# Kernel optimization log

Measured on AMD Instinct MI355X. Metric: run time of the kernel, lower is better.

Reference implementation:

```python
import jax, jax.numpy as jnp
import numpy as np

N_HEAD, N, F_IN, F_OUT = 8, 4096, 128, 128


def setup_inputs() -> dict:
    key = jax.random.key(0)
    k1, k2, k3, k4 = jax.random.split(key, 4)
    return {
        "h": jax.random.normal(k1, (N, F_IN), dtype=jnp.float32),
        "w": jax.random.normal(k2, (N_HEAD, F_IN, F_OUT), dtype=jnp.float32) * 0.1,
        "a_src": jax.random.normal(k3, (N_HEAD, F_OUT, 1), dtype=jnp.float32) * 0.1,
        "a_dst": jax.random.normal(k4, (N_HEAD, F_OUT, 1), dtype=jnp.float32) * 0.1,
        "bias": jnp.zeros((F_OUT,), dtype=jnp.float32),
        "idx": 0,
    }


def reference(h, w, a_src, a_dst, bias, idx):
    # h: [n, f_in], w: [H, f_in, f_out] -> h_prime: [H, n, f_out]
    h_prime = jnp.einsum("ni,hio->hno", h, w)
    # per-node scalar scores per head: [H, n]
    attn_src = jnp.einsum("hno,ho->hn", h_prime, a_src[..., 0])
    attn_dst = jnp.einsum("hno,ho->hn", h_prime, a_dst[..., 0])
    # dense additive attention: [H, n, n] (src broadcast over cols + dst over rows)
    attn = attn_src[:, :, None] + attn_dst[:, None, :]
    attn = jax.nn.leaky_relu(attn, negative_slope=0.2)
    attn = jax.nn.softmax(attn, axis=-1)
    # dropout is identity in eval mode
    out = jnp.einsum("hnm,hmo->hno", attn, h_prime)  # [H, n, f_out]
    return out.mean(axis=0) + bias  # [n, f_out]
```

## Files before the change

### kernel.cpp

```cpp
#include <hip/hip_runtime.h>
#include <math.h>

#define NH 8
#define NN 4096
#define FF 128
#define SEG 32
#define NSEG (NN / SEG)

typedef unsigned long long u64;

__global__ __launch_bounds__(128) void kA_va(
    const float* __restrict__ w, const float* __restrict__ a_src,
    const float* __restrict__ a_dst, float* __restrict__ va_s,
    float* __restrict__ va_d) {
  __shared__ float as[FF], ad[FF];
  const int head = blockIdx.x, i = threadIdx.x;
  as[i] = a_src[head * FF + i];
  ad[i] = a_dst[head * FF + i];
  __syncthreads();
  const float4* wr = reinterpret_cast<const float4*>(w + (size_t)head * FF * FF +
                                                     (size_t)i * FF);
  float s = 0.f, d = 0.f;
  #pragma unroll 8
  for (int q = 0; q < 32; ++q) {
    float4 v = wr[q];
    s += v.x * as[q * 4] + v.y * as[q * 4 + 1] + v.z * as[q * 4 + 2] +
         v.w * as[q * 4 + 3];
    d += v.x * ad[q * 4] + v.y * ad[q * 4 + 1] + v.z * ad[q * 4 + 2] +
         v.w * ad[q * 4 + 3];
  }
  va_s[head * FF + i] = s;
  va_d[head * FF + i] = d;
}

__global__ __launch_bounds__(256) void kB_scores(
    const float* __restrict__ h, const float* __restrict__ va_s,
    const float* __restrict__ va_d, float* __restrict__ attn_src,
    float* __restrict__ attn_dst) {
  __shared__ float sh[32 * 132];
  __shared__ float vs[NH * 132], vd[NH * 132];
  const int r0 = blockIdx.x * 32;
  const int tid = threadIdx.x;
  const float4* hg = reinterpret_cast<const float4*>(h);
  #pragma unroll
  for (int it = 0; it < 4; ++it) {
    int q = tid + it * 256;
    int row = q >> 5, c4 = q & 31;
    float4 v = hg[(size_t)(r0 + row) * 32 + c4];
    float* dst = &sh[row * 132 + c4 * 4];
    dst[0] = v.x; dst[1] = v.y; dst[2] = v.z; dst[3] = v.w;
  }
  for (int q = tid; q < NH * FF; q += 256) {
    int hd = q >> 7, k = q & 127;
    vs[hd * 132 + k] = va_s[q];
    vd[hd * 132 + k] = va_d[q];
  }
  __syncthreads();
  const int row = tid >> 3, head = tid & 7;
  float s = 0.f, d = 0.f;
  const float* hr = &sh[row * 132];
  const float* vsp = &vs[head * 132];
  const float* vdp = &vd[head * 132];
  #pragma unroll 8
  for (int k = 0; k < FF; ++k) {
    float hv = hr[k];
    s += hv * vsp[k];
    d += hv * vdp[k];
  }
  attn_src[head * NN + r0 + row] = s;
  attn_dst[head * NN + r0 + row] = d;
}

__global__ __launch_bounds__(256) void k2a_localsort(
    const float* __restrict__ adst, u64* __restrict__ runs) {
  __shared__ u64 sk[512];
  const int head = blockIdx.y, chunk = blockIdx.x, tid = threadIdx.x;
  const int base = head * NN + chunk * 512;
  for (int i = tid; i < 512; i += 256) {
    unsigned ub = __float_as_uint(adst[base + i]);
    unsigned u = (ub & 0x80000000u) ? ~ub : (ub | 0x80000000u);
    sk[i] = ((u64)u << 32) | (unsigned)(chunk * 512 + i);
  }
  __syncthreads();
  for (int k = 2; k <= 512; k <<= 1) {
    for (int j = k >> 1; j > 0; j >>= 1) {
      for (int t = tid; t < 512; t += 256) {
        int ixj = t ^ j;
        if (ixj > t) {
          u64 a = sk[t], b = sk[ixj];
          bool up = ((t & k) == 0);
          if (up ? (a > b) : (a < b)) { sk[t] = b; sk[ixj] = a; }
        }
      }
      __syncthreads();
    }
  }
  for (int i = tid; i < 512; i += 256) runs[base + i] = sk[i];
}

template <int L, bool FINAL>
__global__ __launch_bounds__(256) void k2m(
    const u64* __restrict__ src, u64* __restrict__ dst,
    float* __restrict__ dsort, int* __restrict__ permd) {
  const int head = blockIdx.y;
  const int i = (blockIdx.x * 256 + threadIdx.x) * 4;
  const u64* S = src + head * NN;
  const int region = i / (2 * L), q0 = i % (2 * L);
  const u64* A = S + region * 2 * L;
  const u64* B = A + L;
  int lo = q0 > L ? q0 - L : 0, hi = q0 < L ? q0 : L;
  while (lo < hi) {
    int mid = (lo + hi) >> 1;
    if (A[mid] < B[q0 - 1 - mid]) lo = mid + 1; else hi = mid;
  }
  int a = lo, b = q0 - lo;
  #pragma unroll
  for (int t = 0; t < 4; ++t) {
    u64 va = a < L ? A[a] : ~0ULL;
    u64 vb = b < L ? B[b] : ~0ULL;
    u64 v;
    if (va < vb) { v = va; ++a; } else { v = vb; ++b; }
    const int q = region * 2 * L + q0 + t;
    if (FINAL) {
      unsigned u = (unsigned)(v >> 32);
      unsigned ub = (u & 0x80000000u) ? (u ^ 0x80000000u) : ~u;
      dsort[head * NN + q] = __uint_as_float(ub);
      permd[head * NN + q] = (int)(v & 0xffffffffu);
    } else {
      dst[head * NN + q] = v;
    }
  }
}

__global__ __launch_bounds__(256) void kD_gemm_seg(
    const float* __restrict__ h, const float* __restrict__ w,
    const float* __restrict__ dsort, const int* __restrict__ permd,
    float* __restrict__ hs, float* __restrict__ segs,
    float* __restrict__ segz) {
  __shared__ float sw[32 * 128];
  __shared__ float hA[32 * 128];
  __shared__ float red[2 * 8 * 128];
  __shared__ float se0[SEG], se1[SEG];
  __shared__ int sp[SEG];
  const int head = blockIdx.y, seg = blockIdx.x;
  const int tid = threadIdx.x;
  const int ty = tid >> 5, tx = tid & 31;
  if (tid < SEG) {
    float dv = dsort[head * NN + seg * SEG + tid];
    se0[tid] = expf(0.2f * dv);
    se1[tid] = expf(dv);
    sp[tid] = permd[head * NN + seg * SEG + tid];
  }
  __syncthreads();
  const float4* hg = reinterpret_cast<const float4*>(h);
  #pragma unroll
  for (int it = 0; it < 4; ++it) {
    int row = tid >> 3, c4 = (tid & 7) + it * 8;
    float4 v = hg[(size_t)sp[row] * 32 + c4];
    float* dst = &hA[row * 128 + c4 * 4];
    dst[0] = v.x; dst[1] = v.y; dst[2] = v.z; dst[3] = v.w;
  }
  float acc[4][4];
  #pragma unroll
  for (int i = 0; i < 4; ++i)
    #pragma unroll
    for (int j = 0; j < 4; ++j) acc[i][j] = 0.f;
  const float4* wg = reinterpret_cast<const float4*>(w + (size_t)head * FF * FF);
  for (int kc = 0; kc < 4; ++kc) {
    const int k0 = kc * 32;
    __syncthreads();
    #pragma unroll
    for (int it = 0; it < 4; ++it) {
      int q = tid + it * 256;
      int krow = q >> 5, c4 = q & 31;
      float4 v = wg[(size_t)(k0 + krow) * 32 + c4];
      float* dst = &sw[krow * 128 + c4 * 4];
      dst[0] = v.x; dst[1] = v.y; dst[2] = v.z; dst[3] = v.w;
    }
    __syncthreads();
    #pragma unroll 8
    for (int kk = 0; kk < 32; ++kk) {
      float4 b4 = *reinterpret_cast<const float4*>(&sw[kk * 128 + tx * 4]);
      #pragma unroll
      for (int ri = 0; ri < 4; ++ri) {
        float av = hA[(ty * 4 + ri) * 128 + k0 + kk];
        acc[ri][0] += av * b4.x;
        acc[ri][1] += av * b4.y;
        acc[ri][2] += av * b4.z;
        acc[ri][3] += av * b4.w;
      }
    }
  }
  float4* hs4 = reinterpret_cast<float4*>(hs);
  #pragma unroll
  for (int ri = 0; ri < 4; ++ri) {
    hs4[((size_t)(head * NN + seg * SEG + ty * 4 + ri)) * 32 + tx] =
        make_float4(acc[ri][0], acc[ri][1], acc[ri][2], acc[ri][3]);
  }
  #pragma unroll
  for (int c = 0; c < 4; ++c) {
    float p0 = 0.f, p1 = 0.f;
    #pragma unroll
    for (int ri = 0; ri < 4; ++ri) {
      int R = ty * 4 + ri;
      p0 += se0[R] * acc[ri][c];
      p1 += se1[R] * acc[ri][c];
    }
    red[ty * 128 + tx * 4 + c] = p0;
    red[1024 + ty * 128 + tx * 4 + c] = p1;
  }
  __syncthreads();
  if (tid < FF) {
    float a0 = 0.f, a1 = 0.f;
    #pragma unroll
    for (int g = 0; g < 8; ++g) {
      a0 += red[g * 128 + tid];
      a1 += red[1024 + g * 128 + tid];
    }
    size_t base = ((size_t)(head * NSEG + seg)) * 2 * FF;
    segs[base + tid] = a0;
    segs[base + FF + tid] = a1;
  }
  if (tid == 0) {
    float z0 = 0.f, z1 = 0.f;
    #pragma unroll
    for (int j = 0; j < SEG; ++j) { z0 += se0[j]; z1 += se1[j]; }
    segz[(head * NSEG + seg) * 2 + 0] = z0;
    segz[(head * NSEG + seg) * 2 + 1] = z1;
  }
}

__global__ __launch_bounds__(256) void k4_thresh(
    const float* __restrict__ attn_src, const float* __restrict__ dsort,
    int* __restrict__ tpos) {
  const int i = blockIdx.x * 256 + threadIdx.x;
  const int head = i >> 12, n = i & (NN - 1);
  const float thr = -attn_src[head * NN + n];
  const float* dp = dsort + head * NN;
  int lo = 0, hi = NN;
  while (lo < hi) {
    int mid = (lo + hi) >> 1;
    if (dp[mid] <= thr) lo = mid + 1; else hi = mid;
  }
  tpos[i] = lo;
}

__global__ __launch_bounds__(128) void kF_prefix(
    const float* __restrict__ hs, const float* __restrict__ dsort,
    const float* __restrict__ segs, const float* __restrict__ segz,
    float* __restrict__ PF, float* __restrict__ PFz) {
  __shared__ float se0[SEG], se1[SEG];
  const int head = blockIdx.y, seg = blockIdx.x;
  const int o = threadIdx.x;
  if (o < SEG) {
    float dv = dsort[head * NN + seg * SEG + o];
    se0[o] = expf(0.2f * dv);
    se1[o] = expf(dv);
  }
  __syncthreads();
  float r0 = 0.f, r1 = 0.f, z0 = 0.f, z1 = 0.f;
  const float* sbase = segs + ((size_t)head * NSEG) * 2 * FF;
  #pragma unroll 8
  for (int k = 0; k < seg; ++k) {
    r0 += sbase[(size_t)k * 2 * FF + o];
    r1 += sbase[(size_t)k * 2 * FF + FF + o];
  }
  #pragma unroll 8
  for (int k = 0; k < seg; ++k) {
    z0 += segz[(head * NSEG + k) * 2 + 0];
    z1 += segz[(head * NSEG + k) * 2 + 1];
  }
  const float* hrow = hs + ((size_t)(head * NN + seg * SEG)) * FF + o;
  #pragma unroll 8
  for (int jj = 0; jj < SEG; ++jj) {
    int j = seg * SEG + jj;
    float hv = hrow[(size_t)jj * FF];
    float e0 = se0[jj], e1 = se1[jj];
    r0 += e0 * hv;
    r1 += e1 * hv;
    z0 += e0;
    z1 += e1;
    size_t pb = ((size_t)(head * NN + j)) * 2 * FF;
    PF[pb + o] = r0;
    PF[pb + FF + o] = r1;
    if (o == 0) {
      PFz[(head * NN + j) * 2 + 0] = z0;
      PFz[(head * NN + j) * 2 + 1] = z1;
    }
  }
}

__global__ __launch_bounds__(128) void k6_out(
    const float* __restrict__ attn_src, const int* __restrict__ tpos,
    const float* __restrict__ PF, const float* __restrict__ PFz,
    const float* __restrict__ bias, float* __restrict__ out) {
  const int n = blockIdx.x, o = threadIdx.x;
  float acc = 0.f;
  #pragma unroll
  for (int head = 0; head < NH; ++head) {
    float s = attn_src[head * NN + n];
    int t = tpos[head * NN + n];
    size_t tb = ((size_t)(head * NN + NN - 1)) * 2 * FF;
    float TotA = PF[tb + FF + o];
    float z1tot = PFz[(head * NN + NN - 1) * 2 + 1];
    float B = 0.f, P1 = 0.f, z0p = 0.f, z1p = 0.f;
    if (t > 0) {
      size_t pb = ((size_t)(head * NN + t - 1)) * 2 * FF;
      B = PF[pb + o];
      P1 = PF[pb + FF + o];
      z0p = PFz[(head * NN + t - 1) * 2 + 0];
      z1p = PFz[(head * NN + t - 1) * 2 + 1];
    }
    float e02s = expf(0.2f * s), es = expf(s);
    float den = e02s * z0p + es * (z1tot - z1p);
    acc += (e02s * B + es * (TotA - P1)) / den;
  }
  out[(size_t)n * FF + o] = 0.125f * acc + bias[o];
}

extern "C" void kernel_launch(void* const* d_in, const int* in_sizes, int n_in,
                              void* d_out, int out_size, void* d_ws,
                              size_t ws_size, hipStream_t stream) {
  const float* h = (const float*)d_in[0];
  const float* w = (const float*)d_in[1];
  const float* a_src = (const float*)d_in[2];
  const float* a_dst = (const float*)d_in[3];
  const float* bias = (const float*)d_in[4];
  float* out = (float*)d_out;

  char* ws = (char*)d_ws;
  size_t off = 0;
  auto alloc = [&](size_t bytes) -> void* {
    void* p = ws + off;
    off += (bytes + 255) & ~(size_t)255;
    return p;
  };
  float* hs = (float*)alloc((size_t)NH * NN * FF * 4);
  float* va_s = (float*)alloc((size_t)NH * FF * 4);
  float* va_d = (float*)alloc((size_t)NH * FF * 4);
  float* asrc = (float*)alloc((size_t)NH * NN * 4);
  float* adst = (float*)alloc((size_t)NH * NN * 4);
  float* dsort = (float*)alloc((size_t)NH * NN * 4);
  int* permd = (int*)alloc((size_t)NH * NN * 4);
  int* tpos = (int*)alloc((size_t)NH * NN * 4);
  float* segs = (float*)alloc((size_t)NH * NSEG * 2 * FF * 4);
  float* segz = (float*)alloc((size_t)NH * NSEG * 2 * 4);
  float* PF = (float*)alloc((size_t)NH * NN * 2 * FF * 4);
  float* PFz = (float*)alloc((size_t)NH * NN * 2 * 4);
  u64* sbuf0 = (u64*)alloc((size_t)NH * NN * 8);
  u64* sbuf1 = (u64*)alloc((size_t)NH * NN * 8);
  (void)ws_size; (void)in_sizes; (void)n_in;

  kA_va<<<NH, 128, 0, stream>>>(w, a_src, a_dst, va_s, va_d);
  kB_scores<<<NN / 32, 256, 0, stream>>>(h, va_s, va_d, asrc, adst);
  k2a_localsort<<<dim3(8, NH), 256, 0, stream>>>(adst, sbuf0);
  k2m<512, false><<<dim3(4, NH), 256, 0, stream>>>(sbuf0, sbuf1, nullptr,
                                                   nullptr);
  k2m<1024, false><<<dim3(4, NH), 256, 0, stream>>>(sbuf1, sbuf0, nullptr,
                                                    nullptr);
  k2m<2048, true><<<dim3(4, NH), 256, 0, stream>>>(sbuf0, nullptr, dsort,
                                                   permd);
  kD_gemm_seg<<<dim3(NSEG, NH), 256, 0, stream>>>(h, w, dsort, permd, hs, segs,
                                                  segz);
  k4_thresh<<<NH * NN / 256, 256, 0, stream>>>(asrc, dsort, tpos);
  kF_prefix<<<dim3(NSEG, NH), 128, 0, stream>>>(hs, dsort, segs, segz, PF,
                                                PFz);
  k6_out<<<NN, 128, 0, stream>>>(asrc, tpos, PF, PFz, bias, out);
}
```

Before: 164.3 us.

## Fuse merge passes into shared-memory kernel and fold threshold search into output

The two global merge-sort passes (512 and 1024 run lengths) are combined into one kernel that merges 2048-element halves in LDS, leaving a single global final merge. The threshold binary search kernel is removed and its work moved into k6_out, where 8 threads per block search dsort for each head and share the result through LDS. This removes two kernel launches and the tpos round trip. In exchange the in-LDS merge runs on only 16 blocks, and the output kernel now waits on a serial binary search before its main loop.

```diff
diff --git a/kernel.cpp b/kernel.cpp
--- a/kernel.cpp
+++ b/kernel.cpp
@@ -98,16 +98,67 @@
   for (int i = tid; i < 512; i += 256) runs[base + i] = sk[i];
 }
 
-template <int L, bool FINAL>
-__global__ __launch_bounds__(256) void k2m(
-    const u64* __restrict__ src, u64* __restrict__ dst,
-    float* __restrict__ dsort, int* __restrict__ permd) {
+__global__ __launch_bounds__(256) void k2b_localmerge(
+    const u64* __restrict__ src, u64* __restrict__ dst) {
+  __shared__ u64 b0[2048], b1[2048];
+  const int head = blockIdx.y, half = blockIdx.x, tid = threadIdx.x;
+  const int base = head * NN + half * 2048;
+  for (int i = tid; i < 2048; i += 256) b0[i] = src[base + i];
+  __syncthreads();
+  {
+    const int q = tid * 8;
+    const int region = q >> 10, q0 = q & 1023;
+    const u64* A = &b0[region << 10];
+    const u64* B = A + 512;
+    int lo = q0 > 512 ? q0 - 512 : 0, hi = q0 < 512 ? q0 : 512;
+    while (lo < hi) {
+      int mid = (lo + hi) >> 1;
+      if (A[mid] < B[q0 - 1 - mid]) lo = mid + 1; else hi = mid;
+    }
+    int a = lo, b = q0 - lo;
+    #pragma unroll
+    for (int t = 0; t < 8; ++t) {
+      u64 va = a < 512 ? A[a] : ~0ULL;
+      u64 vb = b < 512 ? B[b] : ~0ULL;
+      u64 v;
+      if (va < vb) { v = va; ++a; } else { v = vb; ++b; }
+      b1[(region << 10) + q0 + t] = v;
+    }
+  }
+  __syncthreads();
+  {
+    const int q0 = tid * 8;
+    const u64* A = b1;
+    const u64* B = b1 + 1024;
+    int lo = q0 > 1024 ? q0 - 1024 : 0, hi = q0 < 1024 ? q0 : 1024;
+    while (lo < hi) {
+      int mid = (lo + hi) >> 1;
+      if (A[mid] < B[q0 - 1 - mid]) lo = mid + 1; else hi = mid;
+    }
+    int a = lo, b = q0 - lo;
+    #pragma unroll
+    for (int t = 0; t < 8; ++t) {
+      u64 va = a < 1024 ? A[a] : ~0ULL;
+      u64 vb = b < 1024 ? B[b] : ~0ULL;
+      u64 v;
+      if (va < vb) { v = va; ++a; } else { v = vb; ++b; }
+      b0[q0 + t] = v;
+    }
+  }
+  __syncthreads();
+  for (int i = tid; i < 2048; i += 256) dst[base + i] = b0[i];
+}
+
+__global__ __launch_bounds__(256) void k2m_final(
+    const u64* __restrict__ src, float* __restrict__ dsort,
+    int* __restrict__ permd) {
+  const int L = 2048;
   const int head = blockIdx.y;
   const int i = (blockIdx.x * 256 + threadIdx.x) * 4;
   const u64* S = src + head * NN;
-  const int region = i / (2 * L), q0 = i % (2 * L);
-  const u64* A = S + region * 2 * L;
-  const u64* B = A + L;
+  const int q0 = i;
+  const u64* A = S;
+  const u64* B = S + L;
   int lo = q0 > L ? q0 - L : 0, hi = q0 < L ? q0 : L;
   while (lo < hi) {
     int mid = (lo + hi) >> 1;
@@ -120,15 +171,11 @@
     u64 vb = b < L ? B[b] : ~0ULL;
     u64 v;
     if (va < vb) { v = va; ++a; } else { v = vb; ++b; }
-    const int q = region * 2 * L + q0 + t;
-    if (FINAL) {
-      unsigned u = (unsigned)(v >> 32);
-      unsigned ub = (u & 0x80000000u) ? (u ^ 0x80000000u) : ~u;
-      dsort[head * NN + q] = __uint_as_float(ub);
-      permd[head * NN + q] = (int)(v & 0xffffffffu);
-    } else {
-      dst[head * NN + q] = v;
-    }
+    const int q = q0 + t;
+    unsigned u = (unsigned)(v >> 32);
+    unsigned ub = (u & 0x80000000u) ? (u ^ 0x80000000u) : ~u;
+    dsort[head * NN + q] = __uint_as_float(ub);
+    permd[head * NN + q] = (int)(v & 0xffffffffu);
   }
 }
 
@@ -230,21 +277,6 @@
   }
 }
 
-__global__ __launch_bounds__(256) void k4_thresh(
-    const float* __restrict__ attn_src, const float* __restrict__ dsort,
-    int* __restrict__ tpos) {
-  const int i = blockIdx.x * 256 + threadIdx.x;
-  const int head = i >> 12, n = i & (NN - 1);
-  const float thr = -attn_src[head * NN + n];
-  const float* dp = dsort + head * NN;
-  int lo = 0, hi = NN;
-  while (lo < hi) {
-    int mid = (lo + hi) >> 1;
-    if (dp[mid] <= thr) lo = mid + 1; else hi = mid;
-  }
-  tpos[i] = lo;
-}
-
 __global__ __launch_bounds__(128) void kF_prefix(
     const float* __restrict__ hs, const float* __restrict__ dsort,
     const float* __restrict__ segs, const float* __restrict__ segz,
@@ -291,15 +323,30 @@
 }
 
 __global__ __launch_bounds__(128) void k6_out(
-    const float* __restrict__ attn_src, const int* __restrict__ tpos,
+    const float* __restrict__ attn_src, const float* __restrict__ dsort,
     const float* __restrict__ PF, const float* __restrict__ PFz,
     const float* __restrict__ bias, float* __restrict__ out) {
+  __shared__ int st[NH];
+  __shared__ float ss[NH];
   const int n = blockIdx.x, o = threadIdx.x;
+  if (o < NH) {
+    float s = attn_src[o * NN + n];
+    ss[o] = s;
+    const float* dp = dsort + o * NN;
+    float thr = -s;
+    int lo = 0, hi = NN;
+    while (lo < hi) {
+      int mid = (lo + hi) >> 1;
+      if (dp[mid] <= thr) lo = mid + 1; else hi = mid;
+    }
+    st[o] = lo;
+  }
+  __syncthreads();
   float acc = 0.f;
   #pragma unroll
   for (int head = 0; head < NH; ++head) {
-    float s = attn_src[head * NN + n];
-    int t = tpos[head * NN + n];
+    float s = ss[head];
+    int t = st[head];
     size_t tb = ((size_t)(head * NN + NN - 1)) * 2 * FF;
     float TotA = PF[tb + FF + o];
     float z1tot = PFz[(head * NN + NN - 1) * 2 + 1];
@@ -342,7 +389,6 @@
   float* adst = (float*)alloc((size_t)NH * NN * 4);
   float* dsort = (float*)alloc((size_t)NH * NN * 4);
   int* permd = (int*)alloc((size_t)NH * NN * 4);
-  int* tpos = (int*)alloc((size_t)NH * NN * 4);
   float* segs = (float*)alloc((size_t)NH * NSEG * 2 * FF * 4);
   float* segz = (float*)alloc((size_t)NH * NSEG * 2 * 4);
   float* PF = (float*)alloc((size_t)NH * NN * 2 * FF * 4);
@@ -354,16 +400,11 @@
   kA_va<<<NH, 128, 0, stream>>>(w, a_src, a_dst, va_s, va_d);
   kB_scores<<<NN / 32, 256, 0, stream>>>(h, va_s, va_d, asrc, adst);
   k2a_localsort<<<dim3(8, NH), 256, 0, stream>>>(adst, sbuf0);
-  k2m<512, false><<<dim3(4, NH), 256, 0, stream>>>(sbuf0, sbuf1, nullptr,
-                                                   nullptr);
-  k2m<1024, false><<<dim3(4, NH), 256, 0, stream>>>(sbuf1, sbuf0, nullptr,
-                                                    nullptr);
-  k2m<2048, true><<<dim3(4, NH), 256, 0, stream>>>(sbuf0, nullptr, dsort,
-                                                   permd);
+  k2b_localmerge<<<dim3(2, NH), 256, 0, stream>>>(sbuf0, sbuf1);
+  k2m_final<<<dim3(4, NH), 256, 0, stream>>>(sbuf1, dsort, permd);
   kD_gemm_seg<<<dim3(NSEG, NH), 256, 0, stream>>>(h, w, dsort, permd, hs, segs,
                                                   segz);
-  k4_thresh<<<NH * NN / 256, 256, 0, stream>>>(asrc, dsort, tpos);
   kF_prefix<<<dim3(NSEG, NH), 128, 0, stream>>>(hs, dsort, segs, segz, PF,
                                                 PFz);
-  k6_out<<<NN, 128, 0, stream>>>(asrc, tpos, PF, PFz, bias, out);
-}
+  k6_out<<<NN, 128, 0, stream>>>(asrc, dsort, PF, PFz, bias, out);
+}
```

Result: faster. 159.6 us (-2.9%).
